# Kernel optimization log

Hardware: AMD Instinct MI355X
Metric: run time of the kernel (lower is better)

The kernel has to match this reference:

```python
import jax, jax.numpy as jnp
import numpy as np

VOCAB = 50000
EMB = 128
ENC = 128
B = 256
K = 4            # tree arity
DEPTH = 5        # root at depth 0
N_NODES = (K ** (DEPTH + 1) - 1) // (K - 1)  # 1365, BFS order: children of i are K*i+1..K*i+K


def setup_inputs() -> dict:
    key = jax.random.key(0)
    ks = jax.random.split(key, 9)
    s = 0.05
    return {
        "tokens": jax.random.randint(ks[0], (N_NODES, B), 0, VOCAB, dtype=jnp.int32),
        "emb_table": jax.random.normal(ks[1], (VOCAB, EMB), jnp.float32) * s,
        "W_ih": jax.random.normal(ks[2], (3 * ENC, EMB), jnp.float32) * s,
        "W_hh": jax.random.normal(ks[3], (3 * ENC, ENC), jnp.float32) * s,
        "b_ih": jax.random.normal(ks[4], (3 * ENC,), jnp.float32) * s,
        "b_hh": jax.random.normal(ks[5], (3 * ENC,), jnp.float32) * s,
        "sent_weight": jax.random.normal(ks[6], (ENC, ENC), jnp.float32) * s,
        "sent_bias": jax.random.normal(ks[7], (1, ENC), jnp.float32) * s,
        "context_weight": jax.random.normal(ks[8], (ENC, 1), jnp.float32) * s,
    }


def _gru_step(x, h, W_ih, W_hh, b_ih, b_hh):
    # torch.nn.GRU single step: gates ordered (r, z, n)
    gi = x @ W_ih.T + b_ih
    gh = h @ W_hh.T + b_hh
    i_r, i_z, i_n = jnp.split(gi, 3, axis=-1)
    h_r, h_z, h_n = jnp.split(gh, 3, axis=-1)
    r = jax.nn.sigmoid(i_r + h_r)
    z = jax.nn.sigmoid(i_z + h_z)
    n = jnp.tanh(i_n + r * h_n)
    return (1.0 - z) * n + z * h


def _encode(tokens, emb_table, W_ih, W_hh, b_ih, b_hh, sent_weight, sent_bias, context_weight):
    # bottom-up over levels of a full K-ary tree; vectorized over (nodes-in-level, batch)
    level_starts = [(K ** d - 1) // (K - 1) for d in range(DEPTH + 2)]
    bsz = tokens.shape[1]
    outs = []
    child_h = None  # [n_{d+1}, B, ENC] hiddens of the level below, level-local order
    for d in range(DEPTH, -1, -1):
        s, e = level_starts[d], level_starts[d + 1]
        n_d = e - s
        x = emb_table[tokens[s:e]]  # [n_d, B, EMB]
        if child_h is None:
            h0 = jnp.zeros((n_d, bsz, ENC), x.dtype)  # leaves: no children
        else:
            # children of local node j are rows j*K..j*K+K-1 of child_h
            ch = child_h.reshape(n_d, K, bsz, ENC).transpose(1, 0, 2, 3)  # [K, n_d, B, E]
            u = jnp.tanh(jnp.einsum('knbe,ef->knbf', ch, sent_weight) + sent_bias)
            scores = jnp.tanh(jnp.einsum('knbe,eo->knbo', u, context_weight))[..., 0]  # [K, n_d, B]
            alpha = jax.nn.softmax(scores, axis=0)  # softmax over children, per (node, batch)
            h0 = jnp.einsum('knbe,knb->nbe', ch, alpha)
        hn = _gru_step(x, h0, W_ih, W_hh, b_ih, b_hh)  # [n_d, B, E]
        outs.append(hn)
        child_h = hn
    all_h = jnp.concatenate(outs, axis=0)  # [N_NODES, B, E]
    return jnp.max(all_h, axis=0)  # torch.max(node_list, 0)[0]


def reference(tokens, emb_table, W_ih, W_hh, b_ih, b_hh, sent_weight, sent_bias, context_weight):
    return _encode(tokens, emb_table, W_ih, W_hh, b_ih, b_hh,
                   sent_weight, sent_bias, context_weight)
```

## Files before the change

### kernel.cpp

```cpp
#include <hip/hip_runtime.h>
#include <hip/hip_bf16.h>
#include <math.h>

typedef short s8 __attribute__((ext_vector_type(8)));
typedef float f4 __attribute__((ext_vector_type(4)));
typedef unsigned short ushort_t;

__device__ __forceinline__ float fexp2f(float x) { return __builtin_amdgcn_exp2f(x); }
__device__ __forceinline__ float frcpf(float x)  { return __builtin_amdgcn_rcpf(x); }
__device__ __forceinline__ float sigf(float x) {
    return frcpf(1.f + fexp2f(x * -1.44269504f));
}
__device__ __forceinline__ float tanh_f(float x) {
    float e = fexp2f(x * 2.88539008f);
    return 1.f - 2.f * frcpf(e + 1.f);
}
__device__ __forceinline__ unsigned pk2(float a, float b) {
    __hip_bfloat162 r = __float22bfloat162_rn(make_float2(a, b));
    return *(unsigned*)&r;
}
__device__ __forceinline__ float b2f(ushort_t b) {
    return __uint_as_float(((unsigned)b) << 16);
}

#define EMB_N   6400000
#define W_N     49152
#define SW_N    16384
#define CVT_N   (EMB_N + 2 * W_N + SW_N)

__global__ __launch_bounds__(256) void cvt_kernel(
    const float* __restrict__ emb, const float* __restrict__ wih,
    const float* __restrict__ whh, const float* __restrict__ sw,
    ushort_t* __restrict__ embb, ushort_t* __restrict__ wihb,
    ushort_t* __restrict__ whhb, ushort_t* __restrict__ swtb)
{
    int i = (blockIdx.x * 256 + threadIdx.x) * 4;
    if (i >= CVT_N) return;
    if (i < EMB_N) {
        float4 v = *(const float4*)(emb + i);
        uint2 o; o.x = pk2(v.x, v.y); o.y = pk2(v.z, v.w);
        *(uint2*)(embb + i) = o;
    } else if (i < EMB_N + W_N) {
        int j = i - EMB_N;
        float4 v = *(const float4*)(wih + j);
        uint2 o; o.x = pk2(v.x, v.y); o.y = pk2(v.z, v.w);
        *(uint2*)(wihb + j) = o;
    } else if (i < EMB_N + 2 * W_N) {
        int j = i - EMB_N - W_N;
        float4 v = *(const float4*)(whh + j);
        uint2 o; o.x = pk2(v.x, v.y); o.y = pk2(v.z, v.w);
        *(uint2*)(whhb + j) = o;
    } else {
        int j = i - EMB_N - 2 * W_N;
        int f = j >> 7, e0 = j & 127;
        uint2 o;
        o.x = pk2(sw[(e0 + 0) * 128 + f], sw[(e0 + 1) * 128 + f]);
        o.y = pk2(sw[(e0 + 2) * 128 + f], sw[(e0 + 3) * 128 + f]);
        *(uint2*)(swtb + j) = o;
    }
}

__global__ __launch_bounds__(512, 2) void leafgru_mfma(
    const ushort_t* __restrict__ embb, const ushort_t* __restrict__ wihb,
    const float* __restrict__ bih, const float* __restrict__ bhh,
    const ushort_t* __restrict__ swt, const float* __restrict__ sb,
    const float* __restrict__ cw,
    ushort_t* __restrict__ hleaf, float* __restrict__ sleaf)
{
    __shared__ ushort_t xs[128 * 136];
    __shared__ ushort_t hnew[128 * 136];
    __shared__ float scp[8][128];

    const int t = threadIdx.x;
    const int base = blockIdx.x * 128;

    {
        int lr = t >> 2, c0 = (t & 3) * 32;
        const ushort_t* src = embb + (size_t)(base + lr) * 128 + c0;
        ushort_t* dst = &xs[lr * 136 + c0];
        #pragma unroll
        for (int i = 0; i < 4; ++i) *(s8*)(dst + 8 * i) = *(const s8*)(src + 8 * i);
    }

    const int lane = t & 63, w = t >> 6;
    const int quad = lane >> 4, l15 = lane & 15;
    const int gA = w * 16 + l15;
    const int g0 = w * 16 + quad * 4;

    s8 bwi[3][4];
    #pragma unroll
    for (int gm = 0; gm < 3; ++gm) {
        const ushort_t* wp = wihb + (size_t)(gm * 128 + gA) * 128 + quad * 8;
        #pragma unroll
        for (int s = 0; s < 4; ++s) bwi[gm][s] = *(const s8*)(wp + 32 * s);
    }
    float bR[4], bZ[4], biN[4], bhN[4];
    {
        float4 a = *(const float4*)(bih + g0);
        float4 b = *(const float4*)(bhh + g0);
        bR[0] = a.x + b.x; bR[1] = a.y + b.y; bR[2] = a.z + b.z; bR[3] = a.w + b.w;
        float4 c = *(const float4*)(bih + 128 + g0);
        float4 d = *(const float4*)(bhh + 128 + g0);
        bZ[0] = c.x + d.x; bZ[1] = c.y + d.y; bZ[2] = c.z + d.z; bZ[3] = c.w + d.w;
        float4 e = *(const float4*)(bih + 256 + g0);
        float4 f = *(const float4*)(bhh + 256 + g0);
        biN[0] = e.x; biN[1] = e.y; biN[2] = e.z; biN[3] = e.w;
        bhN[0] = f.x; bhN[1] = f.y; bhN[2] = f.z; bhN[3] = f.w;
    }

    __syncthreads();

    #pragma unroll 1
    for (int mt = 0; mt < 8; ++mt) {
        const int row = mt * 16 + l15;
        s8 ax[4];
        const ushort_t* ap = &xs[row * 136 + quad * 8];
        #pragma unroll
        for (int s = 0; s < 4; ++s) ax[s] = *(const s8*)(ap + 32 * s);

        f4 accR = (f4)0.f, accZ = (f4)0.f, accN = (f4)0.f;
        #pragma unroll
        for (int s = 0; s < 4; ++s) {
            accR = __builtin_amdgcn_mfma_f32_16x16x32_bf16(bwi[0][s], ax[s], accR, 0, 0, 0);
            accZ = __builtin_amdgcn_mfma_f32_16x16x32_bf16(bwi[1][s], ax[s], accZ, 0, 0, 0);
            accN = __builtin_amdgcn_mfma_f32_16x16x32_bf16(bwi[2][s], ax[s], accN, 0, 0, 0);
        }
        float hv[4];
        #pragma unroll
        for (int r = 0; r < 4; ++r) {
            float G = fexp2f((accR[r] + bR[r]) * -1.44269504f);
            float rr = frcpf(1.f + G);
            float an = accN[r] + biN[r] + rr * bhN[r];
            float E = fexp2f(an * 2.88539008f);
            float F = fexp2f((accZ[r] + bZ[r]) * -1.44269504f);
            float d = frcpf((E + 1.f) * (1.f + F));
            hv[r] = (E - 1.f) * F * d;
        }
        uint2 ov; ov.x = pk2(hv[0], hv[1]); ov.y = pk2(hv[2], hv[3]);
        *(uint2*)&hnew[row * 136 + g0] = ov;
        *(uint2*)(hleaf + (size_t)(base + row) * 128 + g0) = ov;
    }
    __syncthreads();

    s8 bsw[4];
    {
        const ushort_t* wp = swt + (size_t)gA * 128 + quad * 8;
        #pragma unroll
        for (int s = 0; s < 4; ++s) bsw[s] = *(const s8*)(wp + 32 * s);
    }
    float sb4[4], cw4[4];
    {
        float4 a = *(const float4*)(sb + g0);
        float4 b = *(const float4*)(cw + g0);
        sb4[0] = a.x; sb4[1] = a.y; sb4[2] = a.z; sb4[3] = a.w;
        cw4[0] = b.x; cw4[1] = b.y; cw4[2] = b.z; cw4[3] = b.w;
    }

    #pragma unroll 1
    for (int mt = 0; mt < 8; ++mt) {
        const int crow = mt * 16 + l15;
        s8 a[4];
        const ushort_t* ap = &hnew[crow * 136 + quad * 8];
        #pragma unroll
        for (int s = 0; s < 4; ++s) a[s] = *(const s8*)(ap + 32 * s);

        f4 acc = (f4)0.f;
        #pragma unroll
        for (int s = 0; s < 4; ++s)
            acc = __builtin_amdgcn_mfma_f32_16x16x32_bf16(bsw[s], a[s], acc, 0, 0, 0);

        float part = 0.f;
        #pragma unroll
        for (int r = 0; r < 4; ++r)
            part += tanh_f(acc[r] + sb4[r]) * cw4[r];
        part += __shfl_xor(part, 16);
        part += __shfl_xor(part, 32);
        if (quad == 0) scp[w][crow] = part;
    }
    __syncthreads();

    if (t < 128) {
        float s = 0.f;
        #pragma unroll
        for (int ww = 0; ww < 8; ++ww) s += scp[ww][t];
        sleaf[base + t] = tanh_f(s);
    }
}

__global__ __launch_bounds__(512, 2) void gru_fused(
    const int* __restrict__ tokens, const ushort_t* __restrict__ embb,
    const ushort_t* __restrict__ hleaf, const float* __restrict__ sleaf,
    const ushort_t* __restrict__ wihb, const ushort_t* __restrict__ whhb,
    const float* __restrict__ bih, const float* __restrict__ bhh,
    ushort_t* __restrict__ hbuf, ushort_t* __restrict__ pmaxs)
{
    __shared__ ushort_t xs[128 * 136];
    __shared__ ushort_t hs[128 * 136];

    const int t = threadIdx.x;
    const int base = blockIdx.x * 128;

    const int lane = t & 63, w = t >> 6;
    const int quad = lane >> 4, l15 = lane & 15;
    const int gA = w * 16 + l15;
    const int g0 = w * 16 + quad * 4;

    const int slr = t >> 4;
    const int sc0 = (t & 15) * 8;

    s8 bwi[3][4], bwh[3][4];
    #pragma unroll
    for (int gm = 0; gm < 3; ++gm) {
        const ushort_t* wp = wihb + (size_t)(gm * 128 + gA) * 128 + quad * 8;
        #pragma unroll
        for (int s = 0; s < 4; ++s) bwi[gm][s] = *(const s8*)(wp + 32 * s);
        const ushort_t* wp2 = whhb + (size_t)(gm * 128 + gA) * 128 + quad * 8;
        #pragma unroll
        for (int s = 0; s < 4; ++s) bwh[gm][s] = *(const s8*)(wp2 + 32 * s);
    }
    float bR[4], bZ[4], biN[4], bhN[4];
    {
        float4 a = *(const float4*)(bih + g0);
        float4 b = *(const float4*)(bhh + g0);
        bR[0] = a.x + b.x; bR[1] = a.y + b.y; bR[2] = a.z + b.z; bR[3] = a.w + b.w;
        float4 c = *(const float4*)(bih + 128 + g0);
        float4 d = *(const float4*)(bhh + 128 + g0);
        bZ[0] = c.x + d.x; bZ[1] = c.y + d.y; bZ[2] = c.z + d.z; bZ[3] = c.w + d.w;
        float4 e = *(const float4*)(bih + 256 + g0);
        float4 f = *(const float4*)(bhh + 256 + g0);
        biN[0] = e.x; biN[1] = e.y; biN[2] = e.z; biN[3] = e.w;
        bhN[0] = f.x; bhN[1] = f.y; bhN[2] = f.z; bhN[3] = f.w;
    }

    s8 pv0, pv1, pv2, pv3, pxv;
    float ps0, ps1, ps2, ps3;
    int pnode, pb;

#define STAGE_LOAD(Q) {                                                     \
        int lr_ = (Q) * 32 + slr;                                           \
        int grow_ = base + lr_;                                             \
        pnode = grow_ >> 8; pb = grow_ & 255;                               \
        int lt0 = tokens[(341 + 4 * pnode + 0) * 256 + pb];                 \
        int lt1 = tokens[(341 + 4 * pnode + 1) * 256 + pb];                 \
        int lt2 = tokens[(341 + 4 * pnode + 2) * 256 + pb];                 \
        int lt3 = tokens[(341 + 4 * pnode + 3) * 256 + pb];                 \
        pv0 = *(const s8*)(hleaf + (size_t)lt0 * 128 + sc0);                \
        pv1 = *(const s8*)(hleaf + (size_t)lt1 * 128 + sc0);                \
        pv2 = *(const s8*)(hleaf + (size_t)lt2 * 128 + sc0);                \
        pv3 = *(const s8*)(hleaf + (size_t)lt3 * 128 + sc0);                \
        ps0 = sleaf[lt0]; ps1 = sleaf[lt1]; ps2 = sleaf[lt2]; ps3 = sleaf[lt3]; \
        int tok_ = tokens[(85 + pnode) * 256 + pb];                         \
        pxv = *(const s8*)(embb + (size_t)tok_ * 128 + sc0);                \
    }

#define STAGE_FIN(Q) {                                                      \
        int lr_ = (Q) * 32 + slr;                                           \
        float m_ = fmaxf(fmaxf(ps0, ps1), fmaxf(ps2, ps3));                 \
        float e0_ = fexp2f((ps0 - m_) * 1.44269504f);                       \
        float e1_ = fexp2f((ps1 - m_) * 1.44269504f);                       \
        float e2_ = fexp2f((ps2 - m_) * 1.44269504f);                       \
        float e3_ = fexp2f((ps3 - m_) * 1.44269504f);                       \
        float inv_ = frcpf(e0_ + e1_ + e2_ + e3_);                          \
        float a0_ = e0_ * inv_, a1_ = e1_ * inv_;                           \
        float a2_ = e2_ * inv_, a3_ = e3_ * inv_;                           \
        float o_[8], mm_[8];                                                \
        _Pragma("unroll")                                                   \
        for (int j = 0; j < 8; ++j) {                                       \
            float y0 = b2f((ushort_t)pv0[j]), y1 = b2f((ushort_t)pv1[j]);   \
            float y2 = b2f((ushort_t)pv2[j]), y3 = b2f((ushort_t)pv3[j]);   \
            o_[j]  = a0_ * y0 + a1_ * y1 + a2_ * y2 + a3_ * y3;             \
            mm_[j] = fmaxf(fmaxf(y0, y1), fmaxf(y2, y3));                   \
        }                                                                   \
        uint4 ovv_, mvv_;                                                   \
        ovv_.x = pk2(o_[0], o_[1]);  ovv_.y = pk2(o_[2], o_[3]);            \
        ovv_.z = pk2(o_[4], o_[5]);  ovv_.w = pk2(o_[6], o_[7]);            \
        mvv_.x = pk2(mm_[0], mm_[1]); mvv_.y = pk2(mm_[2], mm_[3]);         \
        mvv_.z = pk2(mm_[4], mm_[5]); mvv_.w = pk2(mm_[6], mm_[7]);         \
        *(uint4*)&hs[lr_ * 136 + sc0] = ovv_;                               \
        *(s8*)&xs[lr_ * 136 + sc0] = pxv;                                   \
        *(uint4*)(pmaxs + ((size_t)pb * 320 + pnode) * 128 + sc0) = mvv_;   \
    }

    STAGE_LOAD(0);
    STAGE_FIN(0);
    __syncthreads();

    #pragma unroll 1
    for (int q = 0; q < 4; ++q) {
        if (q < 3) STAGE_LOAD(q + 1);

        #pragma unroll 1
        for (int mq = 0; mq < 2; ++mq) {
            const int mt = q * 2 + mq;
            const int row = mt * 16 + l15;
            s8 ax[4], ah[4];
            {
                const ushort_t* ap = &xs[row * 136 + quad * 8];
                #pragma unroll
                for (int s = 0; s < 4; ++s) ax[s] = *(const s8*)(ap + 32 * s);
                const ushort_t* hp = &hs[row * 136 + quad * 8];
                #pragma unroll
                for (int s = 0; s < 4; ++s) ah[s] = *(const s8*)(hp + 32 * s);
            }

            f4 accR = (f4)0.f, accZ = (f4)0.f, accN = (f4)0.f, accNh = (f4)0.f;
            #pragma unroll
            for (int s = 0; s < 4; ++s) {
                accR = __builtin_amdgcn_mfma_f32_16x16x32_bf16(bwi[0][s], ax[s], accR, 0, 0, 0);
                accZ = __builtin_amdgcn_mfma_f32_16x16x32_bf16(bwi[1][s], ax[s], accZ, 0, 0, 0);
                accN = __builtin_amdgcn_mfma_f32_16x16x32_bf16(bwi[2][s], ax[s], accN, 0, 0, 0);
            }
            #pragma unroll
            for (int s = 0; s < 4; ++s) {
                accR  = __builtin_amdgcn_mfma_f32_16x16x32_bf16(bwh[0][s], ah[s], accR, 0, 0, 0);
                accZ  = __builtin_amdgcn_mfma_f32_16x16x32_bf16(bwh[1][s], ah[s], accZ, 0, 0, 0);
                accNh = __builtin_amdgcn_mfma_f32_16x16x32_bf16(bwh[2][s], ah[s], accNh, 0, 0, 0);
            }

            float h0v[4];
            {
                short4 h04 = *(const short4*)&hs[row * 136 + g0];
                h0v[0] = b2f((ushort_t)h04.x); h0v[1] = b2f((ushort_t)h04.y);
                h0v[2] = b2f((ushort_t)h04.z); h0v[3] = b2f((ushort_t)h04.w);
            }
            float hv[4];
            #pragma unroll
            for (int r = 0; r < 4; ++r) {
                float G = fexp2f((accR[r] + bR[r]) * -1.44269504f);
                float rr = frcpf(1.f + G);
                float an = accN[r] + biN[r] + rr * (accNh[r] + bhN[r]);
                float E = fexp2f(an * 2.88539008f);
                float F = fexp2f((accZ[r] + bZ[r]) * -1.44269504f);
                float d = frcpf((E + 1.f) * (1.f + F));
                hv[r] = ((E - 1.f) * F + h0v[r] * (E + 1.f)) * d;
            }
            uint2 ov; ov.x = pk2(hv[0], hv[1]); ov.y = pk2(hv[2], hv[3]);
            *(uint2*)(hbuf + (size_t)(base + row) * 128 + g0) = ov;
        }

        if (q < 3) STAGE_FIN(q + 1);
        __syncthreads();
    }
#undef STAGE_LOAD
#undef STAGE_FIN
}

__global__ __launch_bounds__(512, 2) void attnmax_mfma(
    const ushort_t* __restrict__ hch, ushort_t* __restrict__ h0out,
    ushort_t* __restrict__ pmax,
    const ushort_t* __restrict__ swt, const float* __restrict__ sb,
    const float* __restrict__ cw)
{
    __shared__ ushort_t chs[128 * 136];
    __shared__ float scp[8][128];
    __shared__ float sc[128];
    __shared__ float al[4][32];

    const int t = threadIdx.x;
    const int pbase = blockIdx.x * 32;
    const int pnode = pbase >> 8;
    const int b0 = pbase & 255;

    {
        int lr = t >> 2, c0 = (t & 3) * 32;
        int k = lr >> 5, bl = lr & 31;
        const ushort_t* src = hch + ((size_t)(4 * pnode + k) * 256 + b0 + bl) * 128 + c0;
        ushort_t* dst = &chs[lr * 136 + c0];
        #pragma unroll
        for (int i = 0; i < 4; ++i) *(s8*)(dst + 8 * i) = *(const s8*)(src + 8 * i);
    }

    const int lane = t & 63, w = t >> 6;
    const int quad = lane >> 4, l15 = lane & 15;
    const int fA = w * 16 + l15;
    const int f0 = w * 16 + quad * 4;

    s8 bsw[4];
    {
        const ushort_t* wp = swt + (size_t)fA * 128 + quad * 8;
        #pragma unroll
        for (int s = 0; s < 4; ++s) bsw[s] = *(const s8*)(wp + 32 * s);
    }
    float sb4[4], cw4[4];
    {
        float4 a = *(const float4*)(sb + f0);
        float4 b = *(const float4*)(cw + f0);
        sb4[0] = a.x; sb4[1] = a.y; sb4[2] = a.z; sb4[3] = a.w;
        cw4[0] = b.x; cw4[1] = b.y; cw4[2] = b.z; cw4[3] = b.w;
    }
    __syncthreads();

    #pragma unroll 1
    for (int mt = 0; mt < 8; ++mt) {
        const int crow = mt * 16 + l15;
        s8 a[4];
        const ushort_t* ap = &chs[crow * 136 + quad * 8];
        #pragma unroll
        for (int s = 0; s < 4; ++s) a[s] = *(const s8*)(ap + 32 * s);

        f4 acc = (f4)0.f;
        #pragma unroll
        for (int s = 0; s < 4; ++s)
            acc = __builtin_amdgcn_mfma_f32_16x16x32_bf16(bsw[s], a[s], acc, 0, 0, 0);

        float part = 0.f;
        #pragma unroll
        for (int r = 0; r < 4; ++r)
            part += tanh_f(acc[r] + sb4[r]) * cw4[r];
        part += __shfl_xor(part, 16);
        part += __shfl_xor(part, 32);
        if (quad == 0) scp[w][crow] = part;
    }
    __syncthreads();

    if (t < 128) {
        float s = 0.f;
        #pragma unroll
        for (int ww = 0; ww < 8; ++ww) s += scp[ww][t];
        sc[t] = tanh_f(s);
    }
    __syncthreads();

    if (t < 32) {
        float s0 = sc[t], s1 = sc[32 + t], s2 = sc[64 + t], s3 = sc[96 + t];
        float m = fmaxf(fmaxf(s0, s1), fmaxf(s2, s3));
        float e0 = fexp2f((s0 - m) * 1.44269504f), e1 = fexp2f((s1 - m) * 1.44269504f);
        float e2 = fexp2f((s2 - m) * 1.44269504f), e3 = fexp2f((s3 - m) * 1.44269504f);
        float inv = frcpf(e0 + e1 + e2 + e3);
        al[0][t] = e0 * inv; al[1][t] = e1 * inv; al[2][t] = e2 * inv; al[3][t] = e3 * inv;
    }
    __syncthreads();

    {
        int bl = t >> 4, e0 = (t & 15) * 8;
        float a0 = al[0][bl], a1 = al[1][bl], a2 = al[2][bl], a3 = al[3][bl];
        s8 c0v = *(const s8*)&chs[(0 * 32 + bl) * 136 + e0];
        s8 c1v = *(const s8*)&chs[(1 * 32 + bl) * 136 + e0];
        s8 c2v = *(const s8*)&chs[(2 * 32 + bl) * 136 + e0];
        s8 c3v = *(const s8*)&chs[(3 * 32 + bl) * 136 + e0];
        float o[8], m[8];
        #pragma unroll
        for (int j = 0; j < 8; ++j) {
            float x0 = b2f((ushort_t)c0v[j]), x1 = b2f((ushort_t)c1v[j]);
            float x2 = b2f((ushort_t)c2v[j]), x3 = b2f((ushort_t)c3v[j]);
            o[j] = a0 * x0 + a1 * x1 + a2 * x2 + a3 * x3;
            m[j] = fmaxf(fmaxf(x0, x1), fmaxf(x2, x3));
        }
        uint4 ovv, mvv;
        ovv.x = pk2(o[0], o[1]); ovv.y = pk2(o[2], o[3]);
        ovv.z = pk2(o[4], o[5]); ovv.w = pk2(o[6], o[7]);
        mvv.x = pk2(m[0], m[1]); mvv.y = pk2(m[2], m[3]);
        mvv.z = pk2(m[4], m[5]); mvv.w = pk2(m[6], m[7]);
        size_t rh = ((size_t)pnode * 256 + b0 + bl) * 128 + e0;
        *(uint4*)(h0out + rh) = ovv;
        size_t rp = ((size_t)(b0 + bl) * 320 + 256 + pnode) * 128 + e0;
        *(uint4*)(pmax + rp) = mvv;
    }
}

__global__ __launch_bounds__(512, 1) void tail_kernel(
    const int* __restrict__ tokens, const ushort_t* __restrict__ embb,
    const ushort_t* __restrict__ wihb, const ushort_t* __restrict__ whhb,
    const float* __restrict__ bih, const float* __restrict__ bhh,
    const ushort_t* __restrict__ swt, const float* __restrict__ sb,
    const float* __restrict__ cw,
    const ushort_t* __restrict__ h0g,
    const ushort_t* __restrict__ pmax,
    float* __restrict__ out)
{
    __shared__ ushort_t xs[64 * 136];
    __shared__ ushort_t hnew[64 * 136];
    __shared__ ushort_t hs[64 * 136];
    __shared__ float scp[8][64];
    __shared__ float sc[64];
    __shared__ float al[4][16];
    __shared__ float smax[4][128];
    __shared__ float wpart[8][128];

    const int t = threadIdx.x;
    const int bb = blockIdx.x;
    const int lane = t & 63, w = t >> 6;
    const int quad = lane >> 4, l15 = lane & 15;
    const int gA = w * 16 + l15;
    const int g0 = w * 16 + quad * 4;

    s8 bwi[3][4], bwh[3][4];
    #pragma unroll
    for (int gm = 0; gm < 3; ++gm) {
        const ushort_t* wp = wihb + (size_t)(gm * 128 + gA) * 128 + quad * 8;
        #pragma unroll
        for (int s = 0; s < 4; ++s) bwi[gm][s] = *(const s8*)(wp + 32 * s);
        const ushort_t* wp2 = whhb + (size_t)(gm * 128 + gA) * 128 + quad * 8;
        #pragma unroll
        for (int s = 0; s < 4; ++s) bwh[gm][s] = *(const s8*)(wp2 + 32 * s);
    }
    float bR[4], bZ[4], biN[4], bhN[4];
    {
        float4 a = *(const float4*)(bih + g0);
        float4 b = *(const float4*)(bhh + g0);
        bR[0] = a.x + b.x; bR[1] = a.y + b.y; bR[2] = a.z + b.z; bR[3] = a.w + b.w;
        float4 c = *(const float4*)(bih + 128 + g0);
        float4 d = *(const float4*)(bhh + 128 + g0);
        bZ[0] = c.x + d.x; bZ[1] = c.y + d.y; bZ[2] = c.z + d.z; bZ[3] = c.w + d.w;
        float4 e = *(const float4*)(bih + 256 + g0);
        float4 f = *(const float4*)(bhh + 256 + g0);
        biN[0] = e.x; biN[1] = e.y; biN[2] = e.z; biN[3] = e.w;
        bhN[0] = f.x; bhN[1] = f.y; bhN[2] = f.z; bhN[3] = f.w;
    }
    s8 bsw[4];
    {
        const ushort_t* wp = swt + (size_t)gA * 128 + quad * 8;
        #pragma unroll
        for (int s = 0; s < 4; ++s) bsw[s] = *(const s8*)(wp + 32 * s);
    }
    float sb4[4], cw4[4];
    {
        float4 a = *(const float4*)(sb + g0);
        float4 b = *(const float4*)(cw + g0);
        sb4[0] = a.x; sb4[1] = a.y; sb4[2] = a.z; sb4[3] = a.w;
        cw4[0] = b.x; cw4[1] = b.y; cw4[2] = b.z; cw4[3] = b.w;
    }

    float vmax = -INFINITY;

    const int nodesA[4] = {64, 16, 4, 1};
    const int tok0A[4]  = {21, 5, 1, 0};

    #pragma unroll 1
    for (int L = 0; L < 4; ++L) {
        const int nodes = nodesA[L], tok0 = tok0A[L];
        const int R = (nodes < 16) ? 16 : nodes;
        const int mts = R >> 4;

        {
            int lr = t >> 3, c0 = (t & 7) * 16;
            if (lr < R) {
                int n = min(lr, nodes - 1);
                int tok = tokens[(tok0 + n) * 256 + bb];
                const ushort_t* src = embb + (size_t)tok * 128 + c0;
                ushort_t* dst = &xs[lr * 136 + c0];
                *(s8*)(dst)     = *(const s8*)(src);
                *(s8*)(dst + 8) = *(const s8*)(src + 8);
                if (L == 0) {
                    const ushort_t* hsrc = h0g + ((size_t)n * 256 + bb) * 128 + c0;
                    ushort_t* hdst = &hs[lr * 136 + c0];
                    *(s8*)(hdst)     = *(const s8*)(hsrc);
                    *(s8*)(hdst + 8) = *(const s8*)(hsrc + 8);
                }
            }
        }
        __syncthreads();

        for (int mt = 0; mt < mts; ++mt) {
            const int row = mt * 16 + l15;
            const int hr = min(row, nodes - 1);
            s8 ax[4], ah[4];
            {
                const ushort_t* ap = &xs[row * 136 + quad * 8];
                #pragma unroll
                for (int s = 0; s < 4; ++s) ax[s] = *(const s8*)(ap + 32 * s);
                const ushort_t* hp = &hs[hr * 136 + quad * 8];
                #pragma unroll
                for (int s = 0; s < 4; ++s) ah[s] = *(const s8*)(hp + 32 * s);
            }
            f4 accR = (f4)0.f, accZ = (f4)0.f, accN = (f4)0.f, accNh = (f4)0.f;
            #pragma unroll
            for (int s = 0; s < 4; ++s) {
                accR = __builtin_amdgcn_mfma_f32_16x16x32_bf16(bwi[0][s], ax[s], accR, 0, 0, 0);
                accZ = __builtin_amdgcn_mfma_f32_16x16x32_bf16(bwi[1][s], ax[s], accZ, 0, 0, 0);
                accN = __builtin_amdgcn_mfma_f32_16x16x32_bf16(bwi[2][s], ax[s], accN, 0, 0, 0);
            }
            #pragma unroll
            for (int s = 0; s < 4; ++s) {
                accR  = __builtin_amdgcn_mfma_f32_16x16x32_bf16(bwh[0][s], ah[s], accR, 0, 0, 0);
                accZ  = __builtin_amdgcn_mfma_f32_16x16x32_bf16(bwh[1][s], ah[s], accZ, 0, 0, 0);
                accNh = __builtin_amdgcn_mfma_f32_16x16x32_bf16(bwh[2][s], ah[s], accNh, 0, 0, 0);
            }
            float h0v[4];
            {
                short4 h04 = *(const short4*)&hs[hr * 136 + g0];
                h0v[0] = b2f((ushort_t)h04.x); h0v[1] = b2f((ushort_t)h04.y);
                h0v[2] = b2f((ushort_t)h04.z); h0v[3] = b2f((ushort_t)h04.w);
            }
            float hv[4];
            #pragma unroll
            for (int r = 0; r < 4; ++r) {
                float rr = sigf(accR[r] + bR[r]);
                float zz = sigf(accZ[r] + bZ[r]);
                float nn = tanh_f(accN[r] + biN[r] + rr * (accNh[r] + bhN[r]));
                hv[r] = nn + zz * (h0v[r] - nn);
            }
            uint2 ov; ov.x = pk2(hv[0], hv[1]); ov.y = pk2(hv[2], hv[3]);
            *(uint2*)&hnew[row * 136 + g0] = ov;
        }
        __syncthreads();

        {
            int col = t & 127, g = t >> 7;
            for (int r = g; r < R; r += 4)
                vmax = fmaxf(vmax, b2f(hnew[r * 136 + col]));
        }

        if (L < 3) {
            for (int mt = 0; mt < mts; ++mt) {
                const int crow = mt * 16 + l15;
                s8 a[4];
                const ushort_t* ap = &hnew[crow * 136 + quad * 8];
                #pragma unroll
                for (int s = 0; s < 4; ++s) a[s] = *(const s8*)(ap + 32 * s);
                f4 acc = (f4)0.f;
                #pragma unroll
                for (int s = 0; s < 4; ++s)
                    acc = __builtin_amdgcn_mfma_f32_16x16x32_bf16(bsw[s], a[s], acc, 0, 0, 0);
                float part = 0.f;
                #pragma unroll
                for (int r = 0; r < 4; ++r)
                    part += tanh_f(acc[r] + sb4[r]) * cw4[r];
                part += __shfl_xor(part, 16);
                part += __shfl_xor(part, 32);
                if (quad == 0) scp[w][crow] = part;
            }
            __syncthreads();
            if (t < R) {
                float s = 0.f;
                #pragma unroll
                for (int g = 0; g < 8; ++g) s += scp[g][t];
                sc[t] = tanh_f(s);
            }
            __syncthreads();
            const int P = nodes >> 2;
            if (t < P) {
                float s0 = sc[4 * t + 0], s1 = sc[4 * t + 1];
                float s2 = sc[4 * t + 2], s3 = sc[4 * t + 3];
                float m = fmaxf(fmaxf(s0, s1), fmaxf(s2, s3));
                float e0 = fexp2f((s0 - m) * 1.44269504f);
                float e1 = fexp2f((s1 - m) * 1.44269504f);
                float e2 = fexp2f((s2 - m) * 1.44269504f);
                float e3 = fexp2f((s3 - m) * 1.44269504f);
                float inv = frcpf(e0 + e1 + e2 + e3);
                al[0][t] = e0 * inv; al[1][t] = e1 * inv;
                al[2][t] = e2 * inv; al[3][t] = e3 * inv;
            }
            __syncthreads();
            if (t < 16 * P) {
                int bl = t >> 4, e0 = (t & 15) * 8;
                float a0 = al[0][bl], a1 = al[1][bl], a2 = al[2][bl], a3 = al[3][bl];
                s8 c0v = *(const s8*)&hnew[(4 * bl + 0) * 136 + e0];
                s8 c1v = *(const s8*)&hnew[(4 * bl + 1) * 136 + e0];
                s8 c2v = *(const s8*)&hnew[(4 * bl + 2) * 136 + e0];
                s8 c3v = *(const s8*)&hnew[(4 * bl + 3) * 136 + e0];
                float o[8];
                #pragma unroll
                for (int j = 0; j < 8; ++j) {
                    o[j] = a0 * b2f((ushort_t)c0v[j]) + a1 * b2f((ushort_t)c1v[j])
                         + a2 * b2f((ushort_t)c2v[j]) + a3 * b2f((ushort_t)c3v[j]);
                }
                uint4 ovv;
                ovv.x = pk2(o[0], o[1]); ovv.y = pk2(o[2], o[3]);
                ovv.z = pk2(o[4], o[5]); ovv.w = pk2(o[6], o[7]);
                *(uint4*)&hs[bl * 136 + e0] = ovv;
            }
            __syncthreads();
        }
    }

    smax[t >> 7][t & 127] = vmax;

    {
        int cg = t & 15;
        int ck = t >> 4;
        const ushort_t* base = pmax + (size_t)bb * 320 * 128 + cg * 8;
        float v8[8];
        #pragma unroll
        for (int j = 0; j < 8; ++j) v8[j] = -INFINITY;
        for (int s = ck; s < 320; s += 32) {
            s8 c = *(const s8*)(base + (size_t)s * 128);
            #pragma unroll
            for (int j = 0; j < 8; ++j) v8[j] = fmaxf(v8[j], b2f((ushort_t)c[j]));
        }
        #pragma unroll
        for (int j = 0; j < 8; ++j) {
            v8[j] = fmaxf(v8[j], __shfl_xor(v8[j], 16));
            v8[j] = fmaxf(v8[j], __shfl_xor(v8[j], 32));
        }
        if (lane < 16) {
            #pragma unroll
            for (int j = 0; j < 8; ++j) wpart[w][lane * 8 + j] = v8[j];
        }
    }
    __syncthreads();

    if (t < 128) {
        float m = wpart[0][t];
        #pragma unroll
        for (int ww = 1; ww < 8; ++ww) m = fmaxf(m, wpart[ww][t]);
        float own = fmaxf(fmaxf(smax[0][t], smax[1][t]),
                          fmaxf(smax[2][t], smax[3][t]));
        out[(size_t)bb * 128 + t] = fmaxf(m, own);
    }
}

extern "C" void kernel_launch(void* const* d_in, const int* in_sizes, int n_in,
                              void* d_out, int out_size, void* d_ws, size_t ws_size,
                              hipStream_t stream)
{
    const int*   tokens = (const int*)d_in[0];
    const float* emb    = (const float*)d_in[1];
    const float* Wih    = (const float*)d_in[2];
    const float* Whh    = (const float*)d_in[3];
    const float* bih    = (const float*)d_in[4];
    const float* bhh    = (const float*)d_in[5];
    const float* SW     = (const float*)d_in[6];
    const float* sb     = (const float*)d_in[7];
    const float* cw     = (const float*)d_in[8];
    float* out = (float*)d_out;

    ushort_t* embb  = (ushort_t*)d_ws;
    ushort_t* wihb  = embb + (size_t)EMB_N;
    ushort_t* whhb  = wihb + W_N;
    ushort_t* swtb  = whhb + W_N;
    ushort_t* hleaf = swtb + SW_N;
    float*    sleaf = (float*)(hleaf + (size_t)50176 * 128);
    ushort_t* h4    = (ushort_t*)(sleaf + 50176);
    ushort_t* h0_3  = h4 + (size_t)256 * 32768;
    ushort_t* pmax  = h0_3 + (size_t)64 * 32768;

    cvt_kernel<<<(CVT_N / 4 + 255) / 256, 256, 0, stream>>>(
        emb, Wih, Whh, SW, embb, wihb, whhb, swtb);

    leafgru_mfma<<<392, 512, 0, stream>>>(
        embb, wihb, bih, bhh, swtb, sb, cw, hleaf, sleaf);

    gru_fused<<<512, 512, 0, stream>>>(
        tokens, embb, hleaf, sleaf, wihb, whhb, bih, bhh, h4, pmax);

    attnmax_mfma<<<512, 512, 0, stream>>>(h4, h0_3, pmax, swtb, sb, cw);

    tail_kernel<<<256, 512, 0, stream>>>(
        tokens, embb, wihb, whhb, bih, bhh, swtb, sb, cw,
        h0_3, pmax, out);
}
```

Baseline: 181.8 us.

## Precompute per-vocab input-gate projections in leaf kernel and reuse in level-4 GRU

Result: slower. 194.2 us (+6.8%).

```diff
diff --git a/kernel.cpp b/kernel.cpp
--- a/kernel.cpp
+++ b/kernel.cpp
@@ -21,6 +21,10 @@
 }
 __device__ __forceinline__ float b2f(ushort_t b) {
     return __uint_as_float(((unsigned)b) << 16);
+}
+__device__ __forceinline__ void up4(uint2 u, float* v) {
+    v[0] = b2f((ushort_t)(u.x & 0xffff)); v[1] = b2f((ushort_t)(u.x >> 16));
+    v[2] = b2f((ushort_t)(u.y & 0xffff)); v[3] = b2f((ushort_t)(u.y >> 16));
 }
 
 #define EMB_N   6400000
@@ -65,7 +69,8 @@
     const float* __restrict__ bih, const float* __restrict__ bhh,
     const ushort_t* __restrict__ swt, const float* __restrict__ sb,
     const float* __restrict__ cw,
-    ushort_t* __restrict__ hleaf, float* __restrict__ sleaf)
+    ushort_t* __restrict__ hleaf, float* __restrict__ sleaf,
+    ushort_t* __restrict__ gtab)
 {
     __shared__ ushort_t xs[128 * 136];
     __shared__ ushort_t hnew[128 * 136];
@@ -125,6 +130,18 @@
             accZ = __builtin_amdgcn_mfma_f32_16x16x32_bf16(bwi[1][s], ax[s], accZ, 0, 0, 0);
             accN = __builtin_amdgcn_mfma_f32_16x16x32_bf16(bwi[2][s], ax[s], accN, 0, 0, 0);
         }
+
+        {
+            ushort_t* gp = gtab + (size_t)(base + row) * 384 + g0;
+            uint2 gR, gZ, gN;
+            gR.x = pk2(accR[0], accR[1]); gR.y = pk2(accR[2], accR[3]);
+            gZ.x = pk2(accZ[0], accZ[1]); gZ.y = pk2(accZ[2], accZ[3]);
+            gN.x = pk2(accN[0], accN[1]); gN.y = pk2(accN[2], accN[3]);
+            *(uint2*)(gp)       = gR;
+            *(uint2*)(gp + 128) = gZ;
+            *(uint2*)(gp + 256) = gN;
+        }
+
         float hv[4];
         #pragma unroll
         for (int r = 0; r < 4; ++r) {
@@ -188,13 +205,12 @@
 }
 
 __global__ __launch_bounds__(512, 2) void gru_fused(
-    const int* __restrict__ tokens, const ushort_t* __restrict__ embb,
+    const int* __restrict__ tokens,
     const ushort_t* __restrict__ hleaf, const float* __restrict__ sleaf,
-    const ushort_t* __restrict__ wihb, const ushort_t* __restrict__ whhb,
+    const ushort_t* __restrict__ gtab, const ushort_t* __restrict__ whhb,
     const float* __restrict__ bih, const float* __restrict__ bhh,
     ushort_t* __restrict__ hbuf, ushort_t* __restrict__ pmaxs)
 {
-    __shared__ ushort_t xs[128 * 136];
     __shared__ ushort_t hs[128 * 136];
 
     const int t = threadIdx.x;
@@ -208,12 +224,9 @@
     const int slr = t >> 4;
     const int sc0 = (t & 15) * 8;
 
-    s8 bwi[3][4], bwh[3][4];
+    s8 bwh[3][4];
     #pragma unroll
     for (int gm = 0; gm < 3; ++gm) {
-        const ushort_t* wp = wihb + (size_t)(gm * 128 + gA) * 128 + quad * 8;
-        #pragma unroll
-        for (int s = 0; s < 4; ++s) bwi[gm][s] = *(const s8*)(wp + 32 * s);
         const ushort_t* wp2 = whhb + (size_t)(gm * 128 + gA) * 128 + quad * 8;
         #pragma unroll
         for (int s = 0; s < 4; ++s) bwh[gm][s] = *(const s8*)(wp2 + 32 * s);
@@ -232,7 +245,7 @@
         bhN[0] = f.x; bhN[1] = f.y; bhN[2] = f.z; bhN[3] = f.w;
     }
 
-    s8 pv0, pv1, pv2, pv3, pxv;
+    s8 pv0, pv1, pv2, pv3;
     float ps0, ps1, ps2, ps3;
     int pnode, pb;
 
@@ -249,8 +262,6 @@
         pv2 = *(const s8*)(hleaf + (size_t)lt2 * 128 + sc0);                \
         pv3 = *(const s8*)(hleaf + (size_t)lt3 * 128 + sc0);                \
         ps0 = sleaf[lt0]; ps1 = sleaf[lt1]; ps2 = sleaf[lt2]; ps3 = sleaf[lt3]; \
-        int tok_ = tokens[(85 + pnode) * 256 + pb];                         \
-        pxv = *(const s8*)(embb + (size_t)tok_ * 128 + sc0);                \
     }
 
 #define STAGE_FIN(Q) {                                                      \
@@ -277,7 +288,6 @@
         mvv_.x = pk2(mm_[0], mm_[1]); mvv_.y = pk2(mm_[2], mm_[3]);         \
         mvv_.z = pk2(mm_[4], mm_[5]); mvv_.w = pk2(mm_[6], mm_[7]);         \
         *(uint4*)&hs[lr_ * 136 + sc0] = ovv_;                               \
-        *(s8*)&xs[lr_ * 136 + sc0] = pxv;                                   \
         *(uint4*)(pmaxs + ((size_t)pb * 320 + pnode) * 128 + sc0) = mvv_;   \
     }
 
@@ -293,23 +303,23 @@
         for (int mq = 0; mq < 2; ++mq) {
             const int mt = q * 2 + mq;
             const int row = mt * 16 + l15;
-            s8 ax[4], ah[4];
+
+            int grow = base + row;
+            int node = grow >> 8, b = grow & 255;
+            int tok = tokens[(85 + node) * 256 + b];
+            const ushort_t* gp = gtab + (size_t)tok * 384 + g0;
+            uint2 gRu = *(const uint2*)(gp);
+            uint2 gZu = *(const uint2*)(gp + 128);
+            uint2 gNu = *(const uint2*)(gp + 256);
+
+            s8 ah[4];
             {
-                const ushort_t* ap = &xs[row * 136 + quad * 8];
-                #pragma unroll
-                for (int s = 0; s < 4; ++s) ax[s] = *(const s8*)(ap + 32 * s);
                 const ushort_t* hp = &hs[row * 136 + quad * 8];
                 #pragma unroll
                 for (int s = 0; s < 4; ++s) ah[s] = *(const s8*)(hp + 32 * s);
             }
 
-            f4 accR = (f4)0.f, accZ = (f4)0.f, accN = (f4)0.f, accNh = (f4)0.f;
-            #pragma unroll
-            for (int s = 0; s < 4; ++s) {
-                accR = __builtin_amdgcn_mfma_f32_16x16x32_bf16(bwi[0][s], ax[s], accR, 0, 0, 0);
-                accZ = __builtin_amdgcn_mfma_f32_16x16x32_bf16(bwi[1][s], ax[s], accZ, 0, 0, 0);
-                accN = __builtin_amdgcn_mfma_f32_16x16x32_bf16(bwi[2][s], ax[s], accN, 0, 0, 0);
-            }
+            f4 accR = (f4)0.f, accZ = (f4)0.f, accNh = (f4)0.f;
             #pragma unroll
             for (int s = 0; s < 4; ++s) {
                 accR  = __builtin_amdgcn_mfma_f32_16x16x32_bf16(bwh[0][s], ah[s], accR, 0, 0, 0);
@@ -323,14 +333,17 @@
                 h0v[0] = b2f((ushort_t)h04.x); h0v[1] = b2f((ushort_t)h04.y);
                 h0v[2] = b2f((ushort_t)h04.z); h0v[3] = b2f((ushort_t)h04.w);
             }
+            float giR[4], giZ[4], giN[4];
+            up4(gRu, giR); up4(gZu, giZ); up4(gNu, giN);
+
             float hv[4];
             #pragma unroll
             for (int r = 0; r < 4; ++r) {
-                float G = fexp2f((accR[r] + bR[r]) * -1.44269504f);
+                float G = fexp2f((giR[r] + accR[r] + bR[r]) * -1.44269504f);
                 float rr = frcpf(1.f + G);
-                float an = accN[r] + biN[r] + rr * (accNh[r] + bhN[r]);
+                float an = giN[r] + biN[r] + rr * (accNh[r] + bhN[r]);
                 float E = fexp2f(an * 2.88539008f);
-                float F = fexp2f((accZ[r] + bZ[r]) * -1.44269504f);
+                float F = fexp2f((giZ[r] + accZ[r] + bZ[r]) * -1.44269504f);
                 float d = frcpf((E + 1.f) * (1.f + F));
                 hv[r] = ((E - 1.f) * F + h0v[r] * (E + 1.f)) * d;
             }
@@ -721,7 +734,8 @@
     ushort_t* swtb  = whhb + W_N;
     ushort_t* hleaf = swtb + SW_N;
     float*    sleaf = (float*)(hleaf + (size_t)50176 * 128);
-    ushort_t* h4    = (ushort_t*)(sleaf + 50176);
+    ushort_t* gtab  = (ushort_t*)(sleaf + 50176);
+    ushort_t* h4    = gtab + (size_t)50176 * 384;
     ushort_t* h0_3  = h4 + (size_t)256 * 32768;
     ushort_t* pmax  = h0_3 + (size_t)64 * 32768;
 
@@ -729,10 +743,10 @@
         emb, Wih, Whh, SW, embb, wihb, whhb, swtb);
 
     leafgru_mfma<<<392, 512, 0, stream>>>(
-        embb, wihb, bih, bhh, swtb, sb, cw, hleaf, sleaf);
+        embb, wihb, bih, bhh, swtb, sb, cw, hleaf, sleaf, gtab);
 
     gru_fused<<<512, 512, 0, stream>>>(
-        tokens, embb, hleaf, sleaf, wihb, whhb, bih, bhh, h4, pmax);
+        tokens, hleaf, sleaf, gtab, whhb, bih, bhh, h4, pmax);
 
     attnmax_mfma<<<512, 512, 0, stream>>>(h4, h0_3, pmax, swtb, sb, cw);
 
```

## Fuse level-4 GRU with level-3 child attention to keep hiddens in LDS

Applied to the files above, without the earlier changes.

Result: no change. 181.7 us, median of 2 (-0.0%).

```diff
diff --git a/kernel.cpp b/kernel.cpp
--- a/kernel.cpp
+++ b/kernel.cpp
@@ -187,18 +187,24 @@
     }
 }
 
-__global__ __launch_bounds__(512, 2) void gru_fused(
+__global__ __launch_bounds__(512, 2) void gru_attn_l4(
     const int* __restrict__ tokens, const ushort_t* __restrict__ embb,
     const ushort_t* __restrict__ hleaf, const float* __restrict__ sleaf,
     const ushort_t* __restrict__ wihb, const ushort_t* __restrict__ whhb,
     const float* __restrict__ bih, const float* __restrict__ bhh,
-    ushort_t* __restrict__ hbuf, ushort_t* __restrict__ pmaxs)
+    const ushort_t* __restrict__ swt, const float* __restrict__ sb,
+    const float* __restrict__ cw,
+    ushort_t* __restrict__ h0out, ushort_t* __restrict__ pmaxs)
 {
     __shared__ ushort_t xs[128 * 136];
     __shared__ ushort_t hs[128 * 136];
+    __shared__ float scp[8][128];
+    __shared__ float sc[128];
+    __shared__ float al[4][32];
 
     const int t = threadIdx.x;
-    const int base = blockIdx.x * 128;
+    const int p  = blockIdx.x >> 3;
+    const int b0 = (blockIdx.x & 7) * 32;
 
     const int lane = t & 63, w = t >> 6;
     const int quad = lane >> 4, l15 = lane & 15;
@@ -238,8 +244,7 @@
 
 #define STAGE_LOAD(Q) {                                                     \
         int lr_ = (Q) * 32 + slr;                                           \
-        int grow_ = base + lr_;                                             \
-        pnode = grow_ >> 8; pb = grow_ & 255;                               \
+        pnode = 4 * p + (lr_ >> 5); pb = b0 + (lr_ & 31);                   \
         int lt0 = tokens[(341 + 4 * pnode + 0) * 256 + pb];                 \
         int lt1 = tokens[(341 + 4 * pnode + 1) * 256 + pb];                 \
         int lt2 = tokens[(341 + 4 * pnode + 2) * 256 + pb];                 \
@@ -285,6 +290,8 @@
     STAGE_FIN(0);
     __syncthreads();
 
+    uint2 ph[2];
+
     #pragma unroll 1
     for (int q = 0; q < 4; ++q) {
         if (q < 3) STAGE_LOAD(q + 1);
@@ -335,66 +342,42 @@
                 hv[r] = ((E - 1.f) * F + h0v[r] * (E + 1.f)) * d;
             }
             uint2 ov; ov.x = pk2(hv[0], hv[1]); ov.y = pk2(hv[2], hv[3]);
-            *(uint2*)(hbuf + (size_t)(base + row) * 128 + g0) = ov;
+            ph[mq] = ov;
         }
 
         if (q < 3) STAGE_FIN(q + 1);
         __syncthreads();
+
+        #pragma unroll
+        for (int mq = 0; mq < 2; ++mq) {
+            const int row = (q * 2 + mq) * 16 + l15;
+            *(uint2*)&xs[row * 136 + g0] = ph[mq];
+        }
     }
 #undef STAGE_LOAD
 #undef STAGE_FIN
-}
-
-__global__ __launch_bounds__(512, 2) void attnmax_mfma(
-    const ushort_t* __restrict__ hch, ushort_t* __restrict__ h0out,
-    ushort_t* __restrict__ pmax,
-    const ushort_t* __restrict__ swt, const float* __restrict__ sb,
-    const float* __restrict__ cw)
-{
-    __shared__ ushort_t chs[128 * 136];
-    __shared__ float scp[8][128];
-    __shared__ float sc[128];
-    __shared__ float al[4][32];
-
-    const int t = threadIdx.x;
-    const int pbase = blockIdx.x * 32;
-    const int pnode = pbase >> 8;
-    const int b0 = pbase & 255;
-
-    {
-        int lr = t >> 2, c0 = (t & 3) * 32;
-        int k = lr >> 5, bl = lr & 31;
-        const ushort_t* src = hch + ((size_t)(4 * pnode + k) * 256 + b0 + bl) * 128 + c0;
-        ushort_t* dst = &chs[lr * 136 + c0];
-        #pragma unroll
-        for (int i = 0; i < 4; ++i) *(s8*)(dst + 8 * i) = *(const s8*)(src + 8 * i);
-    }
-
-    const int lane = t & 63, w = t >> 6;
-    const int quad = lane >> 4, l15 = lane & 15;
-    const int fA = w * 16 + l15;
-    const int f0 = w * 16 + quad * 4;
+
+    __syncthreads();
 
     s8 bsw[4];
     {
-        const ushort_t* wp = swt + (size_t)fA * 128 + quad * 8;
+        const ushort_t* wp = swt + (size_t)gA * 128 + quad * 8;
         #pragma unroll
         for (int s = 0; s < 4; ++s) bsw[s] = *(const s8*)(wp + 32 * s);
     }
     float sb4[4], cw4[4];
     {
-        float4 a = *(const float4*)(sb + f0);
-        float4 b = *(const float4*)(cw + f0);
+        float4 a = *(const float4*)(sb + g0);
+        float4 b = *(const float4*)(cw + g0);
         sb4[0] = a.x; sb4[1] = a.y; sb4[2] = a.z; sb4[3] = a.w;
         cw4[0] = b.x; cw4[1] = b.y; cw4[2] = b.z; cw4[3] = b.w;
     }
-    __syncthreads();
 
     #pragma unroll 1
     for (int mt = 0; mt < 8; ++mt) {
         const int crow = mt * 16 + l15;
         s8 a[4];
-        const ushort_t* ap = &chs[crow * 136 + quad * 8];
+        const ushort_t* ap = &xs[crow * 136 + quad * 8];
         #pragma unroll
         for (int s = 0; s < 4; ++s) a[s] = *(const s8*)(ap + 32 * s);
 
@@ -434,10 +417,10 @@
     {
         int bl = t >> 4, e0 = (t & 15) * 8;
         float a0 = al[0][bl], a1 = al[1][bl], a2 = al[2][bl], a3 = al[3][bl];
-        s8 c0v = *(const s8*)&chs[(0 * 32 + bl) * 136 + e0];
-        s8 c1v = *(const s8*)&chs[(1 * 32 + bl) * 136 + e0];
-        s8 c2v = *(const s8*)&chs[(2 * 32 + bl) * 136 + e0];
-        s8 c3v = *(const s8*)&chs[(3 * 32 + bl) * 136 + e0];
+        s8 c0v = *(const s8*)&xs[(0 * 32 + bl) * 136 + e0];
+        s8 c1v = *(const s8*)&xs[(1 * 32 + bl) * 136 + e0];
+        s8 c2v = *(const s8*)&xs[(2 * 32 + bl) * 136 + e0];
+        s8 c3v = *(const s8*)&xs[(3 * 32 + bl) * 136 + e0];
         float o[8], m[8];
         #pragma unroll
         for (int j = 0; j < 8; ++j) {
@@ -451,10 +434,10 @@
         ovv.z = pk2(o[4], o[5]); ovv.w = pk2(o[6], o[7]);
         mvv.x = pk2(m[0], m[1]); mvv.y = pk2(m[2], m[3]);
         mvv.z = pk2(m[4], m[5]); mvv.w = pk2(m[6], m[7]);
-        size_t rh = ((size_t)pnode * 256 + b0 + bl) * 128 + e0;
+        size_t rh = ((size_t)p * 256 + b0 + bl) * 128 + e0;
         *(uint4*)(h0out + rh) = ovv;
-        size_t rp = ((size_t)(b0 + bl) * 320 + 256 + pnode) * 128 + e0;
-        *(uint4*)(pmax + rp) = mvv;
+        size_t rp = ((size_t)(b0 + bl) * 320 + 256 + p) * 128 + e0;
+        *(uint4*)(pmaxs + rp) = mvv;
     }
 }
 
@@ -721,8 +704,7 @@
     ushort_t* swtb  = whhb + W_N;
     ushort_t* hleaf = swtb + SW_N;
     float*    sleaf = (float*)(hleaf + (size_t)50176 * 128);
-    ushort_t* h4    = (ushort_t*)(sleaf + 50176);
-    ushort_t* h0_3  = h4 + (size_t)256 * 32768;
+    ushort_t* h0_3  = (ushort_t*)(sleaf + 50176);
     ushort_t* pmax  = h0_3 + (size_t)64 * 32768;
 
     cvt_kernel<<<(CVT_N / 4 + 255) / 256, 256, 0, stream>>>(
@@ -731,10 +713,9 @@
     leafgru_mfma<<<392, 512, 0, stream>>>(
         embb, wihb, bih, bhh, swtb, sb, cw, hleaf, sleaf);
 
-    gru_fused<<<512, 512, 0, stream>>>(
-        tokens, embb, hleaf, sleaf, wihb, whhb, bih, bhh, h4, pmax);
-
-    attnmax_mfma<<<512, 512, 0, stream>>>(h4, h0_3, pmax, swtb, sb, cw);
+    gru_attn_l4<<<512, 512, 0, stream>>>(
+        tokens, embb, hleaf, sleaf, wihb, whhb, bih, bhh,
+        swtb, sb, cw, h0_3, pmax);
 
     tail_kernel<<<256, 512, 0, stream>>>(
         tokens, embb, wihb, whhb, bih, bhh, swtb, sb, cw,
```
